# Optimization experiments

Hardware: AMD Instinct MI355X
Metric: run time of the kernel (lower is better)

The kernel has to match this reference:

```python
import jax, jax.numpy as jnp
import numpy as np

N, E = 50000, 800000
IN_DIM, HEADS, OUT_DIM = 256, 8, 32
NEG_SLOPE = 0.2  # PyG GATConv default leaky_relu slope
LN_EPS = 1e-5


def setup_inputs() -> dict:
    key = jax.random.key(0)
    ks = jax.random.split(key, 8)
    HC = HEADS * OUT_DIM
    x = jax.random.normal(ks[0], (N, IN_DIM), dtype=jnp.float32)
    edge_index = jax.random.randint(ks[1], (2, E), 0, N, dtype=jnp.int32)
    # GATConv params: lin (no bias), att_src/att_dst [H,C], output bias [H*C]
    W = jax.random.normal(ks[2], (IN_DIM, HC), dtype=jnp.float32) / np.sqrt(IN_DIM)
    att_src = jax.random.normal(ks[3], (HEADS, OUT_DIM), dtype=jnp.float32) / np.sqrt(OUT_DIM)
    att_dst = jax.random.normal(ks[4], (HEADS, OUT_DIM), dtype=jnp.float32) / np.sqrt(OUT_DIM)
    bias = jnp.zeros((HC,), dtype=jnp.float32)
    ln_gamma = jnp.ones((HC,), dtype=jnp.float32)
    ln_beta = jnp.zeros((HC,), dtype=jnp.float32)
    return {"x": x, "edge_index": edge_index, "W": W, "att_src": att_src,
            "att_dst": att_dst, "bias": bias, "ln_gamma": ln_gamma, "ln_beta": ln_beta}


def reference(x, edge_index, W, att_src, att_dst, bias, ln_gamma, ln_beta):
    n = x.shape[0]
    # GATConv adds self-loops by default
    loop = jnp.arange(n, dtype=edge_index.dtype)
    src = jnp.concatenate([edge_index[0], loop])  # [E+N]
    dst = jnp.concatenate([edge_index[1], loop])
    h = (x @ W).reshape(n, HEADS, OUT_DIM)              # [N,H,C]
    a_src = jnp.einsum('nhc,hc->nh', h, att_src)        # [N,H]
    a_dst = jnp.einsum('nhc,hc->nh', h, att_dst)
    e = jax.nn.leaky_relu(a_src[src] + a_dst[dst], NEG_SLOPE)  # [E+N,H]
    # segment-softmax over incoming edges of each destination node
    m = jax.ops.segment_max(e, dst, num_segments=n)
    e = jnp.exp(e - m[dst])
    denom = jax.ops.segment_sum(e, dst, num_segments=n)
    alpha = e / (denom[dst] + 1e-16)                    # [E+N,H]
    out = jax.ops.segment_sum(h[src] * alpha[:, :, None], dst, num_segments=n)
    out = out.reshape(n, HEADS * OUT_DIM) + bias        # concat heads + bias
    # LayerNorm(out_dim*heads); dropout is identity in eval
    mu = jnp.mean(out, axis=-1, keepdims=True)
    var = jnp.mean(jnp.square(out - mu), axis=-1, keepdims=True)
    return ln_gamma * (out - mu) * jax.lax.rsqrt(var + LN_EPS) + ln_beta
```

## Files before the change

### kernel.cpp

```cpp
#include <hip/hip_runtime.h>

#define HEADS 8
#define OUT_DIM 32
#define HC 256
#define IN_DIM 256
#define NEG_SLOPE 0.2f
#define LN_EPS 1e-5f
#define CAP 64

typedef __attribute__((ext_vector_type(8))) short bf16x8;
typedef __attribute__((ext_vector_type(4))) float f32x4;

__device__ __forceinline__ unsigned short f2bf(float f) {
    unsigned int u = __float_as_uint(f);
    unsigned int r = u + 0x7FFFu + ((u >> 16) & 1u);
    return (unsigned short)(r >> 16);
}
__device__ __forceinline__ float bf2f(unsigned short u) {
    return __uint_as_float((unsigned int)u << 16);
}

__global__ __launch_bounds__(256) void cast_wT(const float* __restrict__ W,
                                               unsigned short* __restrict__ Wt) {
    __shared__ float tile[64][65];
    const int n0 = (blockIdx.x & 3) * 64;
    const int k0 = (blockIdx.x >> 2) * 64;
    const int t = threadIdx.x;
    const int r = t >> 4;
    const int c = (t & 15) * 4;
#pragma unroll
    for (int j = 0; j < 4; j++) {
        const int kl = r + j * 16;
        const float4 v = *(const float4*)(W + (size_t)(k0 + kl) * HC + n0 + c);
        tile[kl][c + 0] = v.x; tile[kl][c + 1] = v.y;
        tile[kl][c + 2] = v.z; tile[kl][c + 3] = v.w;
    }
    __syncthreads();
#pragma unroll
    for (int j = 0; j < 4; j++) {
        const int nr = r + j * 16;
        ushort4 o;
        o.x = f2bf(tile[c + 0][nr]);
        o.y = f2bf(tile[c + 1][nr]);
        o.z = f2bf(tile[c + 2][nr]);
        o.w = f2bf(tile[c + 3][nr]);
        *(ushort4*)(Wt + (size_t)(n0 + nr) * IN_DIM + k0 + c) = o;
    }
}

__global__ __launch_bounds__(256) void gemm_bf16(const float* __restrict__ X,
                                                 const unsigned short* __restrict__ Wt,
                                                 unsigned short* __restrict__ Hb, int M) {
    __shared__ unsigned short smem[128 * 40 + 256 * 40];
    unsigned short* As = smem;
    unsigned short* Bs = smem + 128 * 40;
    const int t = threadIdx.x;
    const int m0 = blockIdx.x * 128;
    const int w = t >> 6, lane = t & 63;
    const int wr = w >> 1, wn = w & 1;
    const int l16 = lane & 15, quad = lane >> 4;

    f32x4 acc[4][8] = {};

    for (int k0 = 0; k0 < IN_DIM; k0 += 32) {
#pragma unroll
        for (int j = 0; j < 4; j++) {
            const int idx = t + j * 256;
            const int row = idx >> 3;
            const int part = idx & 7;
            float4 v = make_float4(0.f, 0.f, 0.f, 0.f);
            const int gm = m0 + row;
            if (gm < M) v = *(const float4*)(X + (size_t)gm * IN_DIM + k0 + part * 4);
            ushort4 b;
            b.x = f2bf(v.x); b.y = f2bf(v.y); b.z = f2bf(v.z); b.w = f2bf(v.w);
            *(ushort4*)&As[row * 40 + part * 4] = b;
        }
#pragma unroll
        for (int j = 0; j < 4; j++) {
            const int idx = t + j * 256;
            const int n = idx >> 2;
            const int part = idx & 3;
            *(uint4*)&Bs[n * 40 + part * 8] =
                *(const uint4*)(Wt + (size_t)n * IN_DIM + k0 + part * 8);
        }
        __syncthreads();

        bf16x8 af[4];
#pragma unroll
        for (int mi = 0; mi < 4; mi++) {
            const int row = wr * 64 + mi * 16 + l16;
            af[mi] = *(const bf16x8*)&As[row * 40 + quad * 8];
        }
#pragma unroll
        for (int ni = 0; ni < 8; ni++) {
            const int col = wn * 128 + ni * 16 + l16;
            const bf16x8 bfr = *(const bf16x8*)&Bs[col * 40 + quad * 8];
#pragma unroll
            for (int mi = 0; mi < 4; mi++)
                acc[mi][ni] = __builtin_amdgcn_mfma_f32_16x16x32_bf16(af[mi], bfr, acc[mi][ni], 0, 0, 0);
        }
        __syncthreads();
    }

    unsigned short* cbuf = smem + w * 2048;
#pragma unroll
    for (int mi = 0; mi < 4; mi++) {
#pragma unroll
        for (int ni = 0; ni < 8; ni++) {
#pragma unroll
            for (int reg = 0; reg < 4; reg++) {
                cbuf[(quad * 4 + reg) * 128 + ni * 16 + l16] = f2bf(acc[mi][ni][reg]);
            }
        }
        __syncthreads();
#pragma unroll
        for (int j = 0; j < 4; j++) {
            const int q = lane + 64 * j;
            const int r = q >> 4;
            const int cc = q & 15;
            const uint4 v = *(const uint4*)&cbuf[r * 128 + cc * 8];
            const int gm = m0 + wr * 64 + mi * 16 + r;
            if (gm < M)
                *(uint4*)(Hb + (size_t)gm * HC + wn * 128 + cc * 8) = v;
        }
        __syncthreads();
    }
}

__global__ __launch_bounds__(256) void node_att(const unsigned short* __restrict__ Hb,
                                                const float* __restrict__ att_s,
                                                const float* __restrict__ att_d,
                                                float* __restrict__ a_s,
                                                float* __restrict__ a_d, int N) {
    const int lane = threadIdx.x & 63;
    const int node = blockIdx.x * 4 + (threadIdx.x >> 6);
    if (node >= N) return;
    const ushort4 hv = *(const ushort4*)(Hb + (size_t)node * HC + lane * 4);
    const float vx = bf2f(hv.x), vy = bf2f(hv.y), vz = bf2f(hv.z), vw = bf2f(hv.w);
    const float4 s4 = *(const float4*)(att_s + lane * 4);
    const float4 d4 = *(const float4*)(att_d + lane * 4);
    float ps = vx * s4.x + vy * s4.y + vz * s4.z + vw * s4.w;
    float pd = vx * d4.x + vy * d4.y + vz * d4.z + vw * d4.w;
#pragma unroll
    for (int m = 1; m < 8; m <<= 1) {
        ps += __shfl_xor(ps, m);
        pd += __shfl_xor(pd, m);
    }
    if ((lane & 7) == 0) {
        const int hh = lane >> 3;
        a_s[node * HEADS + hh] = ps;
        a_d[node * HEADS + hh] = pd;
    }
}

__global__ __launch_bounds__(256) void bucket_scatter(const int* __restrict__ ei,
                                                      int* __restrict__ cnt,
                                                      int* __restrict__ bucket,
                                                      int E, int N) {
    const int e = blockIdx.x * 256 + threadIdx.x;
    if (e >= E + N) return;
    int s, d;
    if (e < E) { s = ei[e]; d = ei[E + e]; }
    else       { s = d = e - E; }
    int slot = atomicAdd(&cnt[d], 1);
    if (slot < CAP) bucket[(size_t)d * CAP + slot] = s;
}

__global__ __launch_bounds__(256) void csr_agg(const int* __restrict__ cntArr,
                                               const int* __restrict__ bucket,
                                               const unsigned short* __restrict__ Hb,
                                               const float* __restrict__ a_s,
                                               const float* __restrict__ a_d,
                                               const float* __restrict__ bias,
                                               const float* __restrict__ gamma,
                                               const float* __restrict__ beta,
                                               float* __restrict__ out, int N) {
    const int lane = threadIdx.x & 63;
    const int node = blockIdx.x * 4 + (threadIdx.x >> 6);
    if (node >= N) return;
    const int hh = lane >> 3;
    const int base = node * CAP;
    const int cnt  = min(cntArr[node], CAP);
    const float adv = a_d[(size_t)node * HEADS + hh];

    float4 acc = make_float4(0.f, 0.f, 0.f, 0.f);
    float wsum = 0.f;

    int i = 0;
    for (; i + 8 <= cnt; i += 8) {
        const int4 ia = *(const int4*)(bucket + base + i);
        const int4 ib = *(const int4*)(bucket + base + i + 4);
        const int s[8] = {ia.x, ia.y, ia.z, ia.w, ib.x, ib.y, ib.z, ib.w};
        float tl[8];
#pragma unroll
        for (int j = 0; j < 8; j++) tl[j] = a_s[(size_t)s[j] * HEADS + hh] + adv;
        ushort4 hv[8];
#pragma unroll
        for (int j = 0; j < 8; j++) hv[j] = *(const ushort4*)(Hb + (size_t)s[j] * HC + lane * 4);
#pragma unroll
        for (int j = 0; j < 8; j++) {
            const float l = tl[j] > 0.f ? tl[j] : NEG_SLOPE * tl[j];
            const float w = __expf(l);
            acc.x += w * bf2f(hv[j].x); acc.y += w * bf2f(hv[j].y);
            acc.z += w * bf2f(hv[j].z); acc.w += w * bf2f(hv[j].w);
            wsum += w;
        }
    }
    for (; i + 4 <= cnt; i += 4) {
        const int4 ia = *(const int4*)(bucket + base + i);
        const int s[4] = {ia.x, ia.y, ia.z, ia.w};
        float tl[4];
#pragma unroll
        for (int j = 0; j < 4; j++) tl[j] = a_s[(size_t)s[j] * HEADS + hh] + adv;
        ushort4 hv[4];
#pragma unroll
        for (int j = 0; j < 4; j++) hv[j] = *(const ushort4*)(Hb + (size_t)s[j] * HC + lane * 4);
#pragma unroll
        for (int j = 0; j < 4; j++) {
            const float l = tl[j] > 0.f ? tl[j] : NEG_SLOPE * tl[j];
            const float w = __expf(l);
            acc.x += w * bf2f(hv[j].x); acc.y += w * bf2f(hv[j].y);
            acc.z += w * bf2f(hv[j].z); acc.w += w * bf2f(hv[j].w);
            wsum += w;
        }
    }
    for (; i < cnt; i++) {
        const int s = bucket[base + i];
        float l = a_s[(size_t)s * HEADS + hh] + adv;
        l = l > 0.f ? l : NEG_SLOPE * l;
        const float w = __expf(l);
        const ushort4 hv = *(const ushort4*)(Hb + (size_t)s * HC + lane * 4);
        acc.x += w * bf2f(hv.x); acc.y += w * bf2f(hv.y);
        acc.z += w * bf2f(hv.z); acc.w += w * bf2f(hv.w);
        wsum += w;
    }

    const float inv = 1.f / (wsum + 1e-16f);
    const float4 b4 = *(const float4*)(bias + lane * 4);
    float4 v;
    v.x = acc.x * inv + b4.x;
    v.y = acc.y * inv + b4.y;
    v.z = acc.z * inv + b4.z;
    v.w = acc.w * inv + b4.w;

    float s1 = v.x + v.y + v.z + v.w;
#pragma unroll
    for (int m = 1; m < 64; m <<= 1) s1 += __shfl_xor(s1, m);
    const float mu = s1 * (1.f / 256.f);
    const float dx = v.x - mu, dy = v.y - mu, dz = v.z - mu, dw = v.w - mu;
    float sq = dx * dx + dy * dy + dz * dz + dw * dw;
#pragma unroll
    for (int m = 1; m < 64; m <<= 1) sq += __shfl_xor(sq, m);
    const float rs = rsqrtf(sq * (1.f / 256.f) + LN_EPS);
    const float4 g4 = *(const float4*)(gamma + lane * 4);
    const float4 be = *(const float4*)(beta + lane * 4);
    float4 o;
    o.x = g4.x * dx * rs + be.x;
    o.y = g4.y * dy * rs + be.y;
    o.z = g4.z * dz * rs + be.z;
    o.w = g4.w * dw * rs + be.w;
    *(float4*)(out + (size_t)node * HC + lane * 4) = o;
}

extern "C" void kernel_launch(void* const* d_in, const int* in_sizes, int n_in,
                              void* d_out, int out_size, void* d_ws, size_t ws_size,
                              hipStream_t stream) {
    const float* x     = (const float*)d_in[0];
    const int*   ei    = (const int*)d_in[1];
    const float* W     = (const float*)d_in[2];
    const float* att_s = (const float*)d_in[3];
    const float* att_d = (const float*)d_in[4];
    const float* bias  = (const float*)d_in[5];
    const float* gamma = (const float*)d_in[6];
    const float* beta  = (const float*)d_in[7];
    float* out = (float*)d_out;

    const int N = in_sizes[0] / IN_DIM;
    const int E = in_sizes[1] / 2;
    const int tot = E + N;

    unsigned short* Hb = (unsigned short*)d_ws;
    unsigned short* Wt = Hb + (size_t)N * HC;
    float* a_s  = (float*)(Wt + (size_t)IN_DIM * HC);
    float* a_d  = a_s + (size_t)N * HEADS;
    int* cnt    = (int*)(a_d + (size_t)N * HEADS);
    int* bucket = cnt + N;

    hipMemsetAsync(cnt, 0, (size_t)N * sizeof(int), stream);

    bucket_scatter<<<(tot + 255) / 256, 256, 0, stream>>>(ei, cnt, bucket, E, N);
    cast_wT<<<16, 256, 0, stream>>>(W, Wt);
    gemm_bf16<<<(N + 127) / 128, 256, 0, stream>>>(x, Wt, Hb, N);
    node_att<<<(N + 3) / 4, 256, 0, stream>>>(Hb, att_s, att_d, a_s, a_d, N);

    csr_agg<<<(N + 3) / 4, 256, 0, stream>>>(cnt, bucket, Hb, a_s, a_d,
                                             bias, gamma, beta, out, N);
}
```

Measured before the change: 293.7 us.

## Split aggregation edges across half-waves with 16-byte gathers; drop epilogue barriers

The aggregation kernel now has each half-wavefront handle alternate edges, with every lane gathering 8 bf16 channels in one 16-byte load. The two halves are combined with a cross-half shuffle before LayerNorm, and the statistics are rescaled because each value is counted twice. The node attention kernel likewise processes two nodes per wave with 16-byte loads. Block-wide barriers around the GEMM epilogue's per-wave LDS staging are removed. The aim is to raise memory-level parallelism and reduce load instructions and barrier stalls. The cost is masked tail iterations and reliance on wave-level ordering of LDS accesses.

```diff
diff --git a/kernel.cpp b/kernel.cpp
--- a/kernel.cpp
+++ b/kernel.cpp
@@ -112,7 +112,6 @@
                 cbuf[(quad * 4 + reg) * 128 + ni * 16 + l16] = f2bf(acc[mi][ni][reg]);
             }
         }
-        __syncthreads();
 #pragma unroll
         for (int j = 0; j < 4; j++) {
             const int q = lane + 64 * j;
@@ -123,7 +122,6 @@
             if (gm < M)
                 *(uint4*)(Hb + (size_t)gm * HC + wn * 128 + cc * 8) = v;
         }
-        __syncthreads();
     }
 }
 
@@ -133,21 +131,30 @@
                                                 float* __restrict__ a_s,
                                                 float* __restrict__ a_d, int N) {
     const int lane = threadIdx.x & 63;
-    const int node = blockIdx.x * 4 + (threadIdx.x >> 6);
+    const int wv   = threadIdx.x >> 6;
+    const int half = lane >> 5;
+    const int sl   = lane & 31;
+    const int node = blockIdx.x * 8 + wv * 2 + half;
     if (node >= N) return;
-    const ushort4 hv = *(const ushort4*)(Hb + (size_t)node * HC + lane * 4);
-    const float vx = bf2f(hv.x), vy = bf2f(hv.y), vz = bf2f(hv.z), vw = bf2f(hv.w);
-    const float4 s4 = *(const float4*)(att_s + lane * 4);
-    const float4 d4 = *(const float4*)(att_d + lane * 4);
-    float ps = vx * s4.x + vy * s4.y + vz * s4.z + vw * s4.w;
-    float pd = vx * d4.x + vy * d4.y + vz * d4.z + vw * d4.w;
-#pragma unroll
-    for (int m = 1; m < 8; m <<= 1) {
-        ps += __shfl_xor(ps, m);
-        pd += __shfl_xor(pd, m);
-    }
-    if ((lane & 7) == 0) {
-        const int hh = lane >> 3;
+    const int c0 = sl * 8;
+    const int hh = sl >> 2;
+    const uint4 hv = *(const uint4*)(Hb + (size_t)node * HC + c0);
+    float h[8];
+    h[0] = __uint_as_float(hv.x << 16); h[1] = __uint_as_float(hv.x & 0xffff0000u);
+    h[2] = __uint_as_float(hv.y << 16); h[3] = __uint_as_float(hv.y & 0xffff0000u);
+    h[4] = __uint_as_float(hv.z << 16); h[5] = __uint_as_float(hv.z & 0xffff0000u);
+    h[6] = __uint_as_float(hv.w << 16); h[7] = __uint_as_float(hv.w & 0xffff0000u);
+    const float4 s0 = *(const float4*)(att_s + c0);
+    const float4 s1 = *(const float4*)(att_s + c0 + 4);
+    const float4 d0 = *(const float4*)(att_d + c0);
+    const float4 d1 = *(const float4*)(att_d + c0 + 4);
+    float ps = h[0]*s0.x + h[1]*s0.y + h[2]*s0.z + h[3]*s0.w
+             + h[4]*s1.x + h[5]*s1.y + h[6]*s1.z + h[7]*s1.w;
+    float pd = h[0]*d0.x + h[1]*d0.y + h[2]*d0.z + h[3]*d0.w
+             + h[4]*d1.x + h[5]*d1.y + h[6]*d1.z + h[7]*d1.w;
+    ps += __shfl_xor(ps, 1); ps += __shfl_xor(ps, 2);
+    pd += __shfl_xor(pd, 1); pd += __shfl_xor(pd, 2);
+    if ((sl & 3) == 0) {
         a_s[node * HEADS + hh] = ps;
         a_d[node * HEADS + hh] = pd;
     }
@@ -178,88 +185,85 @@
     const int lane = threadIdx.x & 63;
     const int node = blockIdx.x * 4 + (threadIdx.x >> 6);
     if (node >= N) return;
-    const int hh = lane >> 3;
+    const int half = lane >> 5;
+    const int sl   = lane & 31;
+    const int c0   = sl * 8;
+    const int hh   = sl >> 2;
     const int base = node * CAP;
     const int cnt  = min(cntArr[node], CAP);
     const float adv = a_d[(size_t)node * HEADS + hh];
 
-    float4 acc = make_float4(0.f, 0.f, 0.f, 0.f);
+    float acc[8] = {};
     float wsum = 0.f;
 
-    int i = 0;
-    for (; i + 8 <= cnt; i += 8) {
-        const int4 ia = *(const int4*)(bucket + base + i);
-        const int4 ib = *(const int4*)(bucket + base + i + 4);
-        const int s[8] = {ia.x, ia.y, ia.z, ia.w, ib.x, ib.y, ib.z, ib.w};
-        float tl[8];
-#pragma unroll
-        for (int j = 0; j < 8; j++) tl[j] = a_s[(size_t)s[j] * HEADS + hh] + adv;
-        ushort4 hv[8];
-#pragma unroll
-        for (int j = 0; j < 8; j++) hv[j] = *(const ushort4*)(Hb + (size_t)s[j] * HC + lane * 4);
-#pragma unroll
-        for (int j = 0; j < 8; j++) {
+    for (int i = 0; i < cnt; i += 8) {
+        int sv[4];
+#pragma unroll
+        for (int j = 0; j < 4; j++) {
+            const int idx = i + 2 * j + half;
+            const int sraw = bucket[base + idx];
+            sv[j] = (idx < cnt) ? sraw : 0;
+        }
+        float tl[4];
+#pragma unroll
+        for (int j = 0; j < 4; j++) tl[j] = a_s[(size_t)sv[j] * HEADS + hh] + adv;
+        uint4 hv[4];
+#pragma unroll
+        for (int j = 0; j < 4; j++) hv[j] = *(const uint4*)(Hb + (size_t)sv[j] * HC + c0);
+#pragma unroll
+        for (int j = 0; j < 4; j++) {
             const float l = tl[j] > 0.f ? tl[j] : NEG_SLOPE * tl[j];
-            const float w = __expf(l);
-            acc.x += w * bf2f(hv[j].x); acc.y += w * bf2f(hv[j].y);
-            acc.z += w * bf2f(hv[j].z); acc.w += w * bf2f(hv[j].w);
+            const float w = ((i + 2 * j + half) < cnt) ? __expf(l) : 0.f;
             wsum += w;
-        }
-    }
-    for (; i + 4 <= cnt; i += 4) {
-        const int4 ia = *(const int4*)(bucket + base + i);
-        const int s[4] = {ia.x, ia.y, ia.z, ia.w};
-        float tl[4];
-#pragma unroll
-        for (int j = 0; j < 4; j++) tl[j] = a_s[(size_t)s[j] * HEADS + hh] + adv;
-        ushort4 hv[4];
-#pragma unroll
-        for (int j = 0; j < 4; j++) hv[j] = *(const ushort4*)(Hb + (size_t)s[j] * HC + lane * 4);
-#pragma unroll
-        for (int j = 0; j < 4; j++) {
-            const float l = tl[j] > 0.f ? tl[j] : NEG_SLOPE * tl[j];
-            const float w = __expf(l);
-            acc.x += w * bf2f(hv[j].x); acc.y += w * bf2f(hv[j].y);
-            acc.z += w * bf2f(hv[j].z); acc.w += w * bf2f(hv[j].w);
-            wsum += w;
-        }
-    }
-    for (; i < cnt; i++) {
-        const int s = bucket[base + i];
-        float l = a_s[(size_t)s * HEADS + hh] + adv;
-        l = l > 0.f ? l : NEG_SLOPE * l;
-        const float w = __expf(l);
-        const ushort4 hv = *(const ushort4*)(Hb + (size_t)s * HC + lane * 4);
-        acc.x += w * bf2f(hv.x); acc.y += w * bf2f(hv.y);
-        acc.z += w * bf2f(hv.z); acc.w += w * bf2f(hv.w);
-        wsum += w;
-    }
+            acc[0] += w * __uint_as_float(hv[j].x << 16);
+            acc[1] += w * __uint_as_float(hv[j].x & 0xffff0000u);
+            acc[2] += w * __uint_as_float(hv[j].y << 16);
+            acc[3] += w * __uint_as_float(hv[j].y & 0xffff0000u);
+            acc[4] += w * __uint_as_float(hv[j].z << 16);
+            acc[5] += w * __uint_as_float(hv[j].z & 0xffff0000u);
+            acc[6] += w * __uint_as_float(hv[j].w << 16);
+            acc[7] += w * __uint_as_float(hv[j].w & 0xffff0000u);
+        }
+    }
+
+#pragma unroll
+    for (int k = 0; k < 8; k++) acc[k] += __shfl_xor(acc[k], 32);
+    wsum += __shfl_xor(wsum, 32);
 
     const float inv = 1.f / (wsum + 1e-16f);
-    const float4 b4 = *(const float4*)(bias + lane * 4);
-    float4 v;
-    v.x = acc.x * inv + b4.x;
-    v.y = acc.y * inv + b4.y;
-    v.z = acc.z * inv + b4.z;
-    v.w = acc.w * inv + b4.w;
-
-    float s1 = v.x + v.y + v.z + v.w;
+    const float4 b0 = *(const float4*)(bias + c0);
+    const float4 b1 = *(const float4*)(bias + c0 + 4);
+    float v[8];
+    v[0] = acc[0] * inv + b0.x; v[1] = acc[1] * inv + b0.y;
+    v[2] = acc[2] * inv + b0.z; v[3] = acc[3] * inv + b0.w;
+    v[4] = acc[4] * inv + b1.x; v[5] = acc[5] * inv + b1.y;
+    v[6] = acc[6] * inv + b1.z; v[7] = acc[7] * inv + b1.w;
+
+    float s1 = v[0] + v[1] + v[2] + v[3] + v[4] + v[5] + v[6] + v[7];
 #pragma unroll
     for (int m = 1; m < 64; m <<= 1) s1 += __shfl_xor(s1, m);
-    const float mu = s1 * (1.f / 256.f);
-    const float dx = v.x - mu, dy = v.y - mu, dz = v.z - mu, dw = v.w - mu;
-    float sq = dx * dx + dy * dy + dz * dz + dw * dw;
+    const float mu = s1 * (1.f / 512.f);
+    float d[8];
+    float sq = 0.f;
+#pragma unroll
+    for (int k = 0; k < 8; k++) { d[k] = v[k] - mu; sq += d[k] * d[k]; }
 #pragma unroll
     for (int m = 1; m < 64; m <<= 1) sq += __shfl_xor(sq, m);
-    const float rs = rsqrtf(sq * (1.f / 256.f) + LN_EPS);
-    const float4 g4 = *(const float4*)(gamma + lane * 4);
-    const float4 be = *(const float4*)(beta + lane * 4);
+    const float rs = rsqrtf(sq * (1.f / 512.f) + LN_EPS);
+
+    const float e0 = half ? d[4] : d[0];
+    const float e1 = half ? d[5] : d[1];
+    const float e2 = half ? d[6] : d[2];
+    const float e3 = half ? d[7] : d[3];
+    const int co = c0 + half * 4;
+    const float4 g  = *(const float4*)(gamma + co);
+    const float4 be = *(const float4*)(beta + co);
     float4 o;
-    o.x = g4.x * dx * rs + be.x;
-    o.y = g4.y * dy * rs + be.y;
-    o.z = g4.z * dz * rs + be.z;
-    o.w = g4.w * dw * rs + be.w;
-    *(float4*)(out + (size_t)node * HC + lane * 4) = o;
+    o.x = g.x * e0 * rs + be.x;
+    o.y = g.y * e1 * rs + be.y;
+    o.z = g.z * e2 * rs + be.z;
+    o.w = g.w * e3 * rs + be.w;
+    *(float4*)(out + (size_t)node * HC + co) = o;
 }
 
 extern "C" void kernel_launch(void* const* d_in, const int* in_sizes, int n_in,
@@ -291,7 +295,7 @@
     bucket_scatter<<<(tot + 255) / 256, 256, 0, stream>>>(ei, cnt, bucket, E, N);
     cast_wT<<<16, 256, 0, stream>>>(W, Wt);
     gemm_bf16<<<(N + 127) / 128, 256, 0, stream>>>(x, Wt, Hb, N);
-    node_att<<<(N + 3) / 4, 256, 0, stream>>>(Hb, att_s, att_d, a_s, a_d, N);
+    node_att<<<(N + 7) / 8, 256, 0, stream>>>(Hb, att_s, att_d, a_s, a_d, N);
 
     csr_agg<<<(N + 3) / 4, 256, 0, stream>>>(cnt, bucket, Hb, a_s, a_d,
                                              bias, gamma, beta, out, N);
```

New measurement: 293.3 us. Within noise of the previous version (-0.1%).
